# Performance work log

Measured on AMD Instinct MI355X. Metric: run time of the kernel, lower is better.

Reference implementation:

```python
import jax, jax.numpy as jnp
import numpy as np

N, IN, H, M, C, E = 200000, 256, 256, 64, 64, 3200000

def gelu(x):
    # torch F.gelu default is exact (erf) gelu
    return jax.nn.gelu(x, approximate=False)

def setup_inputs() -> dict:
    key = jax.random.key(0)
    ks = jax.random.split(key, 12)
    s = 0.02  # small init scale for weights
    p = lambda k, shape: jax.random.normal(k, shape, jnp.float32) * s
    inp = {
        "x": jax.random.normal(ks[0], (N, IN), jnp.float32),
        "edge_index": jax.random.randint(ks[1], (2, E), 0, N),
        "ff1_w0": p(ks[2], (IN, H)),   "ff1_b0": jnp.zeros((H,), jnp.float32),
        "wA0":    p(ks[3], (H, H)),    "wB0":    p(ks[4], (H, M)),
        "ff2_w0": p(ks[5], (2 * H, H)),"ff2_b0": jnp.zeros((H,), jnp.float32),
        "ff1_w1": p(ks[6], (H, H)),    "ff1_b1": jnp.zeros((H,), jnp.float32),
        "wA1":    p(ks[7], (H, H)),    "wB1":    p(ks[8], (H, M)),
        "ff2_w1": p(ks[9], (2 * H, H)),"ff2_b1": jnp.zeros((H,), jnp.float32),
        "head_w": p(ks[10], (H, C)),   "head_b": jnp.zeros((C,), jnp.float32),
    }
    return inp

def _ghm_block(X, ff1_w, ff1_b, wA, wB, ff2_w, ff2_b):
    # FF1
    Hf = gelu(X @ ff1_w + ff1_b)                 # (N, h)
    # HyperAggregation: hypernetwork produces token-mixing weights
    W_tar = gelu(Hf @ wA) @ wB                   # (N, m)
    agg = gelu(Hf.T @ W_tar)                     # (h, m) - mixes over nodes
    agg = (agg @ W_tar.T).T                      # (N, h)
    # root connection: concat aggregated with pre-agg features
    agg = gelu(jnp.concatenate([agg, Hf], axis=1))  # (N, 2h)
    return agg @ ff2_w + ff2_b                   # (N, h)

def reference(x, edge_index, ff1_w0, ff1_b0, wA0, wB0, ff2_w0, ff2_b0,
              ff1_w1, ff1_b1, wA1, wB1, ff2_w1, ff2_b1, head_w, head_b):
    # task='graph', batch=None: whole node set is one fully-connected neighborhood
    X = _ghm_block(x, ff1_w0, ff1_b0, wA0, wB0, ff2_w0, ff2_b0)
    X = _ghm_block(X, ff1_w1, ff1_b1, wA1, wB1, ff2_w1, ff2_b1)
    g = jnp.mean(X, axis=0, keepdims=True)       # (1, h)
    return g @ head_w + head_b                   # (1, C)
```

## Files before the change

### kernel.cpp

```cpp
#include <hip/hip_runtime.h>


typedef unsigned short u16;
typedef unsigned int u32;
typedef short bf16x8 __attribute__((ext_vector_type(8)));
typedef float f32x4 __attribute__((ext_vector_type(4)));

__device__ __forceinline__ float gelu_f(float x) {
  float s = x * x;
  float z = x * fmaf(s, -0.10294348f, -2.3022077f);
  float e = __builtin_amdgcn_exp2f(z);
  return x * __builtin_amdgcn_rcpf(1.0f + e);
}
__device__ __forceinline__ u16 f2b(float f) {
  union { float f; unsigned u; } v; v.f = f;
  unsigned u = v.u;
  u += 0x7fffu + ((u >> 16) & 1u);
  return (u16)(u >> 16);
}
__device__ __forceinline__ int swz(int row, int col) {
  return row * 256 + (((col >> 3) ^ (row & 7)) << 3) + (col & 7);
}

__global__ __launch_bounds__(256) void prep_weights(
    const float* __restrict__ s0, const float* __restrict__ s1,
    const float* __restrict__ s2, const float* __restrict__ s3,
    const float* __restrict__ s4, const float* __restrict__ s5,
    const float* __restrict__ s6, const float* __restrict__ s7,
    u16* __restrict__ dst)
{
  int idx = blockIdx.x * 256 + threadIdx.x;
  if (idx >= 557056) return;
  const float* src; int base, R, C;
  if (idx < 278528) {
    if (idx < 131072) {
      if (idx < 65536) { base = 0;      src = s0; R = 256; C = 256; }
      else             { base = 65536;  src = s1; R = 256; C = 256; }
    } else {
      if (idx < 147456){ base = 131072; src = s2; R = 256; C = 64;  }
      else             { base = 147456; src = s3; R = 512; C = 256; }
    }
  } else {
    int j = idx - 278528;
    if (j < 131072) {
      if (j < 65536)   { base = 278528; src = s4; R = 256; C = 256; }
      else             { base = 344064; src = s5; R = 256; C = 256; }
    } else {
      if (j < 147456)  { base = 409600; src = s6; R = 256; C = 64;  }
      else             { base = 425984; src = s7; R = 512; C = 256; }
    }
  }
  int local = idx - base;
  int o = local / R;
  int k = local - o * R;
  dst[idx] = f2b(src[k * C + o]);
}

template<bool AFP32>
__global__ __launch_bounds__(256, 2) void ff1_hyper(
    const void* __restrict__ Av, const u16* __restrict__ W1T,
    const float* __restrict__ bias, const u16* __restrict__ wAT,
    const u16* __restrict__ wBT, u16* __restrict__ Hf,
    u16* __restrict__ Hfg, u16* __restrict__ Wt, int N)
{
  __shared__ u16 Asm[128][264];
  const int tid = threadIdx.x;
  const int wave = tid >> 6, lane = tid & 63;
  int r0 = blockIdx.x * 128;
  if (r0 > N - 128) r0 = N - 128;

  if constexpr (AFP32) {
    const float* A = (const float*)Av;
    #pragma unroll
    for (int j = 0; j < 32; ++j) {
      int idx = j * 256 + tid;
      int row = idx >> 6, c4 = idx & 63;
      float4 v = *(const float4*)(A + (size_t)(r0 + row) * 256 + c4 * 4);
      uint2 p;
      p.x = (u32)f2b(v.x) | ((u32)f2b(v.y) << 16);
      p.y = (u32)f2b(v.z) | ((u32)f2b(v.w) << 16);
      *(uint2*)&Asm[row][c4 * 4] = p;
    }
  } else {
    const u16* A = (const u16*)Av;
    #pragma unroll
    for (int j = 0; j < 16; ++j) {
      int idx = j * 256 + tid;
      int row = idx >> 5, c8 = idx & 31;
      *(uint4*)&Asm[row][c8 * 8] =
          *(const uint4*)(A + (size_t)(r0 + row) * 256 + c8 * 8);
    }
  }
  __syncthreads();

  const int lm = lane & 15, lq = lane >> 4;
  const int n0 = wave * 64;

  f32x4 acc[8][4] = {};
  {
    bf16x8 bb[2][4];
    #pragma unroll
    for (int ct = 0; ct < 4; ++ct)
      bb[0][ct] = *(const bf16x8*)(W1T + (size_t)(n0 + ct * 16 + lm) * 256 + lq * 8);
    #pragma unroll
    for (int s = 0; s < 8; ++s) {
      const int cur = s & 1;
      if (s < 7)
        #pragma unroll
        for (int ct = 0; ct < 4; ++ct)
          bb[cur ^ 1][ct] = *(const bf16x8*)(W1T + (size_t)(n0 + ct * 16 + lm) * 256 + (s + 1) * 32 + lq * 8);
      bf16x8 a[8];
      #pragma unroll
      for (int rt = 0; rt < 8; ++rt)
        a[rt] = *(const bf16x8*)&Asm[rt * 16 + lm][s * 32 + lq * 8];
      #pragma unroll
      for (int rt = 0; rt < 8; ++rt)
        #pragma unroll
        for (int ct = 0; ct < 4; ++ct)
          acc[rt][ct] = __builtin_amdgcn_mfma_f32_16x16x32_bf16(a[rt], bb[cur][ct], acc[rt][ct], 0, 0, 0);
    }
  }
  __syncthreads();
  {
    float bv[4];
    #pragma unroll
    for (int ct = 0; ct < 4; ++ct) bv[ct] = bias[n0 + ct * 16 + lm];
    #pragma unroll
    for (int rt = 0; rt < 8; ++rt)
      #pragma unroll
      for (int ct = 0; ct < 4; ++ct)
        #pragma unroll
        for (int rg = 0; rg < 4; ++rg) {
          float g = gelu_f(acc[rt][ct][rg] + bv[ct]);
          u16 gb = f2b(g);
          int row = rt * 16 + lq * 4 + rg, col = n0 + ct * 16 + lm;
          size_t idx = (size_t)(r0 + row) * 256 + col;
          Hf[idx] = gb;
          Hfg[idx] = f2b(gelu_f(g));
          Asm[row][col] = gb;
        }
  }
  __syncthreads();

  #pragma unroll
  for (int rt = 0; rt < 8; ++rt)
    #pragma unroll
    for (int ct = 0; ct < 4; ++ct)
      acc[rt][ct] = (f32x4){0.f, 0.f, 0.f, 0.f};
  {
    bf16x8 bb[2][4];
    #pragma unroll
    for (int ct = 0; ct < 4; ++ct)
      bb[0][ct] = *(const bf16x8*)(wAT + (size_t)(n0 + ct * 16 + lm) * 256 + lq * 8);
    #pragma unroll
    for (int s = 0; s < 8; ++s) {
      const int cur = s & 1;
      if (s < 7)
        #pragma unroll
        for (int ct = 0; ct < 4; ++ct)
          bb[cur ^ 1][ct] = *(const bf16x8*)(wAT + (size_t)(n0 + ct * 16 + lm) * 256 + (s + 1) * 32 + lq * 8);
      bf16x8 a[8];
      #pragma unroll
      for (int rt = 0; rt < 8; ++rt)
        a[rt] = *(const bf16x8*)&Asm[rt * 16 + lm][s * 32 + lq * 8];
      #pragma unroll
      for (int rt = 0; rt < 8; ++rt)
        #pragma unroll
        for (int ct = 0; ct < 4; ++ct)
          acc[rt][ct] = __builtin_amdgcn_mfma_f32_16x16x32_bf16(a[rt], bb[cur][ct], acc[rt][ct], 0, 0, 0);
    }
  }
  __syncthreads();
  #pragma unroll
  for (int rt = 0; rt < 8; ++rt)
    #pragma unroll
    for (int ct = 0; ct < 4; ++ct)
      #pragma unroll
      for (int rg = 0; rg < 4; ++rg)
        Asm[rt * 16 + lq * 4 + rg][n0 + ct * 16 + lm] = f2b(gelu_f(acc[rt][ct][rg]));
  __syncthreads();

  f32x4 acc2[2][4] = {};
  {
    bf16x8 bb[2][4];
    #pragma unroll
    for (int ct = 0; ct < 4; ++ct)
      bb[0][ct] = *(const bf16x8*)(wBT + (size_t)(ct * 16 + lm) * 256 + lq * 8);
    #pragma unroll
    for (int s = 0; s < 8; ++s) {
      const int cur = s & 1;
      if (s < 7)
        #pragma unroll
        for (int ct = 0; ct < 4; ++ct)
          bb[cur ^ 1][ct] = *(const bf16x8*)(wBT + (size_t)(ct * 16 + lm) * 256 + (s + 1) * 32 + lq * 8);
      bf16x8 a[2];
      #pragma unroll
      for (int rt = 0; rt < 2; ++rt)
        a[rt] = *(const bf16x8*)&Asm[wave * 32 + rt * 16 + lm][s * 32 + lq * 8];
      #pragma unroll
      for (int rt = 0; rt < 2; ++rt)
        #pragma unroll
        for (int ct = 0; ct < 4; ++ct)
          acc2[rt][ct] = __builtin_amdgcn_mfma_f32_16x16x32_bf16(a[rt], bb[cur][ct], acc2[rt][ct], 0, 0, 0);
    }
  }
  #pragma unroll
  for (int rt = 0; rt < 2; ++rt)
    #pragma unroll
    for (int ct = 0; ct < 4; ++ct)
      #pragma unroll
      for (int rg = 0; rg < 4; ++rg)
        Wt[(size_t)(r0 + wave * 32 + rt * 16 + lq * 4 + rg) * 64 + ct * 16 + lm] =
            f2b(acc2[rt][ct][rg]);
}

__global__ __launch_bounds__(256) void s_partial_v2(
    const u16* __restrict__ Hf, const u16* __restrict__ Wt,
    float* __restrict__ Spart, int N)
{
  __shared__ u16 HfT[256][72];
  __shared__ u16 WtT[64][72];
  const int tid = threadIdx.x;
  const int wave = tid >> 6, lane = tid & 63;
  const int lm = lane & 15, lq = lane >> 4;
  const int rp = tid & 31;
  const int mb = tid >> 5;
  uint4 hx[4][2], wx[2];
  auto issue = [&](int ch) {
    int i0 = ch << 6;
    #pragma unroll
    for (int q = 0; q < 4; ++q) {
      const u16* px = Hf + (size_t)(i0 + 2 * rp) * 256 + (mb + 8 * q) * 8;
      hx[q][0] = *(const uint4*)px;
      hx[q][1] = *(const uint4*)(px + 256);
    }
    const u16* pw = Wt + (size_t)(i0 + 2 * rp) * 64 + mb * 8;
    wx[0] = *(const uint4*)pw;
    wx[1] = *(const uint4*)(pw + 64);
  };
  f32x4 acc[4][4] = {};
  const int nchunk = N >> 6;
  int ch = blockIdx.x;
  if (ch < nchunk) issue(ch);
  for (; ch < nchunk; ch += gridDim.x) {
    __syncthreads();
    #pragma unroll
    for (int q = 0; q < 4; ++q) {
      int m = mb + 8 * q;
      u32 xs[4] = {hx[q][0].x, hx[q][0].y, hx[q][0].z, hx[q][0].w};
      u32 ys[4] = {hx[q][1].x, hx[q][1].y, hx[q][1].z, hx[q][1].w};
      #pragma unroll
      for (int t = 0; t < 4; ++t) {
        *(u32*)&HfT[m * 8 + 2 * t][2 * rp]     = (xs[t] & 0xFFFFu) | (ys[t] << 16);
        *(u32*)&HfT[m * 8 + 2 * t + 1][2 * rp] = (xs[t] >> 16) | (ys[t] & 0xFFFF0000u);
      }
    }
    {
      u32 xs[4] = {wx[0].x, wx[0].y, wx[0].z, wx[0].w};
      u32 ys[4] = {wx[1].x, wx[1].y, wx[1].z, wx[1].w};
      #pragma unroll
      for (int t = 0; t < 4; ++t) {
        *(u32*)&WtT[mb * 8 + 2 * t][2 * rp]     = (xs[t] & 0xFFFFu) | (ys[t] << 16);
        *(u32*)&WtT[mb * 8 + 2 * t + 1][2 * rp] = (xs[t] >> 16) | (ys[t] & 0xFFFF0000u);
      }
    }
    __syncthreads();
    if (ch + (int)gridDim.x < nchunk) issue(ch + (int)gridDim.x);
    #pragma unroll
    for (int k0 = 0; k0 < 64; k0 += 32) {
      bf16x8 a[4], b[4];
      #pragma unroll
      for (int t = 0; t < 4; ++t)
        a[t] = *(const bf16x8*)&HfT[wave * 64 + t * 16 + lm][k0 + lq * 8];
      #pragma unroll
      for (int m = 0; m < 4; ++m)
        b[m] = *(const bf16x8*)&WtT[m * 16 + lm][k0 + lq * 8];
      #pragma unroll
      for (int t = 0; t < 4; ++t)
        #pragma unroll
        for (int m = 0; m < 4; ++m)
          acc[t][m] = __builtin_amdgcn_mfma_f32_16x16x32_bf16(a[t], b[m], acc[t][m], 0, 0, 0);
    }
  }
  float* out = Spart + (size_t)blockIdx.x * 16384;
  #pragma unroll
  for (int t = 0; t < 4; ++t)
    #pragma unroll
    for (int m = 0; m < 4; ++m)
      #pragma unroll
      for (int rg = 0; rg < 4; ++rg)
        out[(size_t)(wave * 64 + t * 16 + lq * 4 + rg) * 64 + m * 16 + lm] = acc[t][m][rg];
}

__global__ __launch_bounds__(256) void s_reduce(
    const float* __restrict__ Spart, u16* __restrict__ agg, int nparts)
{
  int e = blockIdx.x * 256 + threadIdx.x;
  float s0 = 0.f, s1 = 0.f, s2 = 0.f, s3 = 0.f;
  for (int p = 0; p < nparts; p += 4) {
    s0 += Spart[(size_t)(p + 0) * 16384 + e];
    s1 += Spart[(size_t)(p + 1) * 16384 + e];
    s2 += Spart[(size_t)(p + 2) * 16384 + e];
    s3 += Spart[(size_t)(p + 3) * 16384 + e];
  }
  agg[e] = f2b(gelu_f((s0 + s1) + (s2 + s3)));
}

template<bool COLSUM>
__global__ __launch_bounds__(256, 2) void fused_p_ff2_v6(
    const u16* __restrict__ Wt, const u16* __restrict__ agg,
    const u16* __restrict__ Hfg, const u16* __restrict__ W2T,
    const float* __restrict__ bias, u16* __restrict__ X,
    float* __restrict__ colsum, int N)
{
  __shared__ u16 Hsm[64 * 256];
  __shared__ u16 Pl[64 * 256];
  const int tid = threadIdx.x;
  const int wave = tid >> 6, lane = tid & 63;
  const int lm = lane & 15, lq = lane >> 4;
  const int r0 = blockIdx.x * 64;
  const int n0 = wave * 64;

  #pragma unroll
  for (int t = 0; t < 8; ++t) {
    int unit = (wave * 8 + t) * 64 + lane;
    int row = unit >> 5, ksw = unit & 31;
    int kc = ksw ^ (row & 7);
    const u16* g = Hfg + (size_t)(r0 + row) * 256 + kc * 8;
    __builtin_amdgcn_global_load_lds(
        (const __attribute__((address_space(1))) void*)g,
        (__attribute__((address_space(3))) void*)(Hsm + (size_t)(wave * 8 + t) * 512),
        16, 0, 0);
  }

  {
    f32x4 acc[4][4] = {};
    #pragma unroll
    for (int k0 = 0; k0 < 64; k0 += 32) {
      bf16x8 a[4], b[4];
      #pragma unroll
      for (int ct = 0; ct < 4; ++ct)
        b[ct] = *(const bf16x8*)(agg + (size_t)(n0 + ct * 16 + lm) * 64 + k0 + lq * 8);
      #pragma unroll
      for (int rt = 0; rt < 4; ++rt)
        a[rt] = *(const bf16x8*)(Wt + (size_t)(r0 + rt * 16 + lm) * 64 + k0 + lq * 8);
      #pragma unroll
      for (int rt = 0; rt < 4; ++rt)
        #pragma unroll
        for (int ct = 0; ct < 4; ++ct)
          acc[rt][ct] = __builtin_amdgcn_mfma_f32_16x16x32_bf16(a[rt], b[ct], acc[rt][ct], 0, 0, 0);
    }
    #pragma unroll
    for (int rt = 0; rt < 4; ++rt)
      #pragma unroll
      for (int ct = 0; ct < 4; ++ct)
        #pragma unroll
        for (int rg = 0; rg < 4; ++rg)
          Pl[swz(rt * 16 + lq * 4 + rg, n0 + ct * 16 + lm)] = f2b(gelu_f(acc[rt][ct][rg]));
  }
  __syncthreads();

  auto ldb = [&](int s, bf16x8* b) {
    #pragma unroll
    for (int ct = 0; ct < 4; ++ct)
      b[ct] = *(const bf16x8*)(W2T + (size_t)(n0 + ct * 16 + lm) * 512 + s * 32 + lq * 8);
  };
  auto lda = [&](int s, bf16x8* a) {
    const u16* base = (s < 8) ? Pl : Hsm;
    const int k0 = (s & 7) * 32;
    #pragma unroll
    for (int rt = 0; rt < 4; ++rt) {
      int row = rt * 16 + lm;
      a[rt] = *(const bf16x8*)&base[swz(row, k0 + lq * 8)];
    }
  };
  f32x4 acc[4][4] = {};
  bf16x8 ab[2][4], bb[2][4];
  ldb(0, bb[0]);
  lda(0, ab[0]);
  #pragma unroll
  for (int s = 0; s < 16; ++s) {
    const int cur = s & 1, nxt = cur ^ 1;
    if (s < 15) { ldb(s + 1, bb[nxt]); lda(s + 1, ab[nxt]); }
    #pragma unroll
    for (int rt = 0; rt < 4; ++rt)
      #pragma unroll
      for (int ct = 0; ct < 4; ++ct)
        acc[rt][ct] = __builtin_amdgcn_mfma_f32_16x16x32_bf16(ab[cur][rt], bb[cur][ct], acc[rt][ct], 0, 0, 0);
  }
  float bv[4];
  #pragma unroll
  for (int ct = 0; ct < 4; ++ct) bv[ct] = bias[n0 + ct * 16 + lm];
  if constexpr (!COLSUM) {
    #pragma unroll
    for (int rt = 0; rt < 4; ++rt)
      #pragma unroll
      for (int ct = 0; ct < 4; ++ct)
        #pragma unroll
        for (int rg = 0; rg < 4; ++rg)
          X[(size_t)(r0 + rt * 16 + lq * 4 + rg) * 256 + n0 + ct * 16 + lm] =
              f2b(acc[rt][ct][rg] + bv[ct]);
  } else {
    #pragma unroll
    for (int ct = 0; ct < 4; ++ct) {
      float cs = 0.0f;
      #pragma unroll
      for (int rt = 0; rt < 4; ++rt)
        #pragma unroll
        for (int rg = 0; rg < 4; ++rg) cs += acc[rt][ct][rg] + bv[ct];
      cs += __shfl_down(cs, 32);
      cs += __shfl_down(cs, 16);
      if (lq == 0) atomicAdd(&colsum[n0 + ct * 16 + lm], cs);
    }
  }
}

__global__ __launch_bounds__(64) void head_kernel(
    const float* __restrict__ colsum, const float* __restrict__ head_w,
    const float* __restrict__ head_b, float* __restrict__ out, float invN)
{
  const int c = threadIdx.x;
  float s = head_b[c];
  for (int h = 0; h < 256; ++h) s = fmaf(colsum[h] * invN, head_w[h * 64 + c], s);
  out[c] = s;
}

extern "C" void kernel_launch(void* const* d_in, const int* in_sizes, int n_in,
                              void* d_out, int out_size, void* d_ws, size_t ws_size,
                              hipStream_t stream)
{
  const float* x        = (const float*)d_in[0];
  const float* ff1_w[2] = {(const float*)d_in[2],  (const float*)d_in[8]};
  const float* ff1_b[2] = {(const float*)d_in[3],  (const float*)d_in[9]};
  const float* wA[2]    = {(const float*)d_in[4],  (const float*)d_in[10]};
  const float* wB[2]    = {(const float*)d_in[5],  (const float*)d_in[11]};
  const float* ff2_w[2] = {(const float*)d_in[6],  (const float*)d_in[12]};
  const float* ff2_b[2] = {(const float*)d_in[7],  (const float*)d_in[13]};
  const float* head_w   = (const float*)d_in[14];
  const float* head_b   = (const float*)d_in[15];
  const int N = in_sizes[0] / 256;

  char* ws = (char*)d_ws;
  u16* WT = (u16*)ws;
  u16* W1T[2] = {WT + 0,      WT + 278528};
  u16* wAT[2] = {WT + 65536,  WT + 344064};
  u16* wBT[2] = {WT + 131072, WT + 409600};
  u16* W2T[2] = {WT + 147456, WT + 425984};
  size_t o = 1114112;
  u16* Hf  = (u16*)(ws + o); o += (size_t)N * 256 * 2;
  u16* Hfg = (u16*)(ws + o); o += (size_t)N * 256 * 2;
  u16* TX  = (u16*)(ws + o); o += (size_t)N * 256 * 2;
  u16* Wt  = (u16*)(ws + o); o += (size_t)N * 64 * 2;
  float* Spart  = (float*)(ws + o); o += (size_t)512 * 16384 * 4;
  u16*   agg    = (u16*)(ws + o);   o += 16384 * 2;
  float* colsum = (float*)(ws + o); o += 256 * 4;
  (void)ws_size; (void)n_in; (void)out_size;

  hipMemsetAsync(colsum, 0, 256 * sizeof(float), stream);
  prep_weights<<<2176, 256, 0, stream>>>(ff1_w[0], wA[0], wB[0], ff2_w[0],
                                         ff1_w[1], wA[1], wB[1], ff2_w[1], WT);
  const int G128 = (N + 127) / 128;
  const int G64  = N / 64;
  ff1_hyper<true><<<G128, 256, 0, stream>>>(x, W1T[0], ff1_b[0], wAT[0], wBT[0], Hf, Hfg, Wt, N);
  s_partial_v2<<<512, 256, 0, stream>>>(Hf, Wt, Spart, N);
  s_reduce<<<64, 256, 0, stream>>>(Spart, agg, 512);
  fused_p_ff2_v6<false><<<G64, 256, 0, stream>>>(Wt, agg, Hfg, W2T[0], ff2_b[0], TX, nullptr, N);
  ff1_hyper<false><<<G128, 256, 0, stream>>>(TX, W1T[1], ff1_b[1], wAT[1], wBT[1], Hf, Hfg, Wt, N);
  s_partial_v2<<<512, 256, 0, stream>>>(Hf, Wt, Spart, N);
  s_reduce<<<64, 256, 0, stream>>>(Spart, agg, 512);
  fused_p_ff2_v6<true><<<G64, 256, 0, stream>>>(Wt, agg, Hfg, W2T[1], ff2_b[1], nullptr, colsum, N);
  head_kernel<<<1, 64, 0, stream>>>(colsum, head_w, head_b, (float*)d_out, 1.0f / (float)N);
}
```

Measured before the change: 1.221 ms.

## Fuse Hf^T·W_tar partial reduction into FF1/hyper kernel, drop Hf buffer

```diff
diff --git a/kernel.cpp b/kernel.cpp
--- a/kernel.cpp
+++ b/kernel.cpp
@@ -57,239 +57,188 @@
 }
 
 template<bool AFP32>
-__global__ __launch_bounds__(256, 2) void ff1_hyper(
+__global__ __launch_bounds__(256, 2) void ff1_hyper_s(
     const void* __restrict__ Av, const u16* __restrict__ W1T,
     const float* __restrict__ bias, const u16* __restrict__ wAT,
-    const u16* __restrict__ wBT, u16* __restrict__ Hf,
-    u16* __restrict__ Hfg, u16* __restrict__ Wt, int N)
-{
-  __shared__ u16 Asm[128][264];
-  const int tid = threadIdx.x;
-  const int wave = tid >> 6, lane = tid & 63;
-  int r0 = blockIdx.x * 128;
-  if (r0 > N - 128) r0 = N - 128;
-
-  if constexpr (AFP32) {
-    const float* A = (const float*)Av;
-    #pragma unroll
-    for (int j = 0; j < 32; ++j) {
-      int idx = j * 256 + tid;
-      int row = idx >> 6, c4 = idx & 63;
-      float4 v = *(const float4*)(A + (size_t)(r0 + row) * 256 + c4 * 4);
-      uint2 p;
-      p.x = (u32)f2b(v.x) | ((u32)f2b(v.y) << 16);
-      p.y = (u32)f2b(v.z) | ((u32)f2b(v.w) << 16);
-      *(uint2*)&Asm[row][c4 * 4] = p;
-    }
-  } else {
-    const u16* A = (const u16*)Av;
-    #pragma unroll
-    for (int j = 0; j < 16; ++j) {
-      int idx = j * 256 + tid;
-      int row = idx >> 5, c8 = idx & 31;
-      *(uint4*)&Asm[row][c8 * 8] =
-          *(const uint4*)(A + (size_t)(r0 + row) * 256 + c8 * 8);
-    }
-  }
-  __syncthreads();
-
-  const int lm = lane & 15, lq = lane >> 4;
-  const int n0 = wave * 64;
-
-  f32x4 acc[8][4] = {};
-  {
-    bf16x8 bb[2][4];
-    #pragma unroll
-    for (int ct = 0; ct < 4; ++ct)
-      bb[0][ct] = *(const bf16x8*)(W1T + (size_t)(n0 + ct * 16 + lm) * 256 + lq * 8);
-    #pragma unroll
-    for (int s = 0; s < 8; ++s) {
-      const int cur = s & 1;
-      if (s < 7)
-        #pragma unroll
-        for (int ct = 0; ct < 4; ++ct)
-          bb[cur ^ 1][ct] = *(const bf16x8*)(W1T + (size_t)(n0 + ct * 16 + lm) * 256 + (s + 1) * 32 + lq * 8);
-      bf16x8 a[8];
-      #pragma unroll
-      for (int rt = 0; rt < 8; ++rt)
-        a[rt] = *(const bf16x8*)&Asm[rt * 16 + lm][s * 32 + lq * 8];
-      #pragma unroll
-      for (int rt = 0; rt < 8; ++rt)
-        #pragma unroll
-        for (int ct = 0; ct < 4; ++ct)
-          acc[rt][ct] = __builtin_amdgcn_mfma_f32_16x16x32_bf16(a[rt], bb[cur][ct], acc[rt][ct], 0, 0, 0);
-    }
-  }
-  __syncthreads();
-  {
-    float bv[4];
-    #pragma unroll
-    for (int ct = 0; ct < 4; ++ct) bv[ct] = bias[n0 + ct * 16 + lm];
-    #pragma unroll
-    for (int rt = 0; rt < 8; ++rt)
-      #pragma unroll
-      for (int ct = 0; ct < 4; ++ct)
-        #pragma unroll
-        for (int rg = 0; rg < 4; ++rg) {
-          float g = gelu_f(acc[rt][ct][rg] + bv[ct]);
-          u16 gb = f2b(g);
-          int row = rt * 16 + lq * 4 + rg, col = n0 + ct * 16 + lm;
-          size_t idx = (size_t)(r0 + row) * 256 + col;
-          Hf[idx] = gb;
-          Hfg[idx] = f2b(gelu_f(g));
-          Asm[row][col] = gb;
-        }
-  }
-  __syncthreads();
-
-  #pragma unroll
-  for (int rt = 0; rt < 8; ++rt)
-    #pragma unroll
-    for (int ct = 0; ct < 4; ++ct)
-      acc[rt][ct] = (f32x4){0.f, 0.f, 0.f, 0.f};
-  {
-    bf16x8 bb[2][4];
-    #pragma unroll
-    for (int ct = 0; ct < 4; ++ct)
-      bb[0][ct] = *(const bf16x8*)(wAT + (size_t)(n0 + ct * 16 + lm) * 256 + lq * 8);
-    #pragma unroll
-    for (int s = 0; s < 8; ++s) {
-      const int cur = s & 1;
-      if (s < 7)
-        #pragma unroll
-        for (int ct = 0; ct < 4; ++ct)
-          bb[cur ^ 1][ct] = *(const bf16x8*)(wAT + (size_t)(n0 + ct * 16 + lm) * 256 + (s + 1) * 32 + lq * 8);
-      bf16x8 a[8];
-      #pragma unroll
-      for (int rt = 0; rt < 8; ++rt)
-        a[rt] = *(const bf16x8*)&Asm[rt * 16 + lm][s * 32 + lq * 8];
-      #pragma unroll
-      for (int rt = 0; rt < 8; ++rt)
-        #pragma unroll
-        for (int ct = 0; ct < 4; ++ct)
-          acc[rt][ct] = __builtin_amdgcn_mfma_f32_16x16x32_bf16(a[rt], bb[cur][ct], acc[rt][ct], 0, 0, 0);
-    }
-  }
-  __syncthreads();
-  #pragma unroll
-  for (int rt = 0; rt < 8; ++rt)
-    #pragma unroll
-    for (int ct = 0; ct < 4; ++ct)
-      #pragma unroll
-      for (int rg = 0; rg < 4; ++rg)
-        Asm[rt * 16 + lq * 4 + rg][n0 + ct * 16 + lm] = f2b(gelu_f(acc[rt][ct][rg]));
-  __syncthreads();
-
-  f32x4 acc2[2][4] = {};
-  {
-    bf16x8 bb[2][4];
-    #pragma unroll
-    for (int ct = 0; ct < 4; ++ct)
-      bb[0][ct] = *(const bf16x8*)(wBT + (size_t)(ct * 16 + lm) * 256 + lq * 8);
-    #pragma unroll
-    for (int s = 0; s < 8; ++s) {
-      const int cur = s & 1;
-      if (s < 7)
-        #pragma unroll
-        for (int ct = 0; ct < 4; ++ct)
-          bb[cur ^ 1][ct] = *(const bf16x8*)(wBT + (size_t)(ct * 16 + lm) * 256 + (s + 1) * 32 + lq * 8);
-      bf16x8 a[2];
-      #pragma unroll
-      for (int rt = 0; rt < 2; ++rt)
-        a[rt] = *(const bf16x8*)&Asm[wave * 32 + rt * 16 + lm][s * 32 + lq * 8];
-      #pragma unroll
-      for (int rt = 0; rt < 2; ++rt)
-        #pragma unroll
-        for (int ct = 0; ct < 4; ++ct)
-          acc2[rt][ct] = __builtin_amdgcn_mfma_f32_16x16x32_bf16(a[rt], bb[cur][ct], acc2[rt][ct], 0, 0, 0);
-    }
-  }
-  #pragma unroll
-  for (int rt = 0; rt < 2; ++rt)
-    #pragma unroll
-    for (int ct = 0; ct < 4; ++ct)
-      #pragma unroll
-      for (int rg = 0; rg < 4; ++rg)
-        Wt[(size_t)(r0 + wave * 32 + rt * 16 + lq * 4 + rg) * 64 + ct * 16 + lm] =
-            f2b(acc2[rt][ct][rg]);
-}
-
-__global__ __launch_bounds__(256) void s_partial_v2(
-    const u16* __restrict__ Hf, const u16* __restrict__ Wt,
-    float* __restrict__ Spart, int N)
-{
-  __shared__ u16 HfT[256][72];
+    const u16* __restrict__ wBT, u16* __restrict__ Hfg,
+    u16* __restrict__ Wt, float* __restrict__ Spart, int N)
+{
+  __shared__ u16 Asm[64][264];
+  __shared__ u16 Tsm[64][264];
   __shared__ u16 WtT[64][72];
   const int tid = threadIdx.x;
   const int wave = tid >> 6, lane = tid & 63;
   const int lm = lane & 15, lq = lane >> 4;
-  const int rp = tid & 31;
-  const int mb = tid >> 5;
-  uint4 hx[4][2], wx[2];
-  auto issue = [&](int ch) {
-    int i0 = ch << 6;
-    #pragma unroll
-    for (int q = 0; q < 4; ++q) {
-      const u16* px = Hf + (size_t)(i0 + 2 * rp) * 256 + (mb + 8 * q) * 8;
-      hx[q][0] = *(const uint4*)px;
-      hx[q][1] = *(const uint4*)(px + 256);
-    }
-    const u16* pw = Wt + (size_t)(i0 + 2 * rp) * 64 + mb * 8;
-    wx[0] = *(const uint4*)pw;
-    wx[1] = *(const uint4*)(pw + 64);
-  };
-  f32x4 acc[4][4] = {};
-  const int nchunk = N >> 6;
-  int ch = blockIdx.x;
-  if (ch < nchunk) issue(ch);
-  for (; ch < nchunk; ch += gridDim.x) {
-    __syncthreads();
-    #pragma unroll
-    for (int q = 0; q < 4; ++q) {
-      int m = mb + 8 * q;
-      u32 xs[4] = {hx[q][0].x, hx[q][0].y, hx[q][0].z, hx[q][0].w};
-      u32 ys[4] = {hx[q][1].x, hx[q][1].y, hx[q][1].z, hx[q][1].w};
-      #pragma unroll
-      for (int t = 0; t < 4; ++t) {
-        *(u32*)&HfT[m * 8 + 2 * t][2 * rp]     = (xs[t] & 0xFFFFu) | (ys[t] << 16);
-        *(u32*)&HfT[m * 8 + 2 * t + 1][2 * rp] = (xs[t] >> 16) | (ys[t] & 0xFFFF0000u);
-      }
-    }
+  const int n0 = wave * 64;
+  const int ntiles = N >> 6;
+
+  float bv[4];
+  #pragma unroll
+  for (int ct = 0; ct < 4; ++ct) bv[ct] = bias[n0 + ct * 16 + lm];
+
+  f32x4 accS[4][4] = {};
+
+  for (int tile = blockIdx.x; tile < ntiles; tile += (int)gridDim.x) {
+    const int r0 = tile << 6;
+
+    if constexpr (AFP32) {
+      const float* A = (const float*)Av;
+      #pragma unroll
+      for (int j = 0; j < 16; ++j) {
+        int idx = j * 256 + tid;
+        int row = idx >> 6, c4 = idx & 63;
+        float4 v = *(const float4*)(A + (size_t)(r0 + row) * 256 + c4 * 4);
+        uint2 p;
+        p.x = (u32)f2b(v.x) | ((u32)f2b(v.y) << 16);
+        p.y = (u32)f2b(v.z) | ((u32)f2b(v.w) << 16);
+        *(uint2*)&Asm[row][c4 * 4] = p;
+      }
+    } else {
+      const u16* A = (const u16*)Av;
+      #pragma unroll
+      for (int j = 0; j < 8; ++j) {
+        int idx = j * 256 + tid;
+        int row = idx >> 5, c8 = idx & 31;
+        *(uint4*)&Asm[row][c8 * 8] =
+            *(const uint4*)(A + (size_t)(r0 + row) * 256 + c8 * 8);
+      }
+    }
+    __syncthreads();
+
+    f32x4 acc[4][4] = {};
     {
-      u32 xs[4] = {wx[0].x, wx[0].y, wx[0].z, wx[0].w};
-      u32 ys[4] = {wx[1].x, wx[1].y, wx[1].z, wx[1].w};
-      #pragma unroll
-      for (int t = 0; t < 4; ++t) {
-        *(u32*)&WtT[mb * 8 + 2 * t][2 * rp]     = (xs[t] & 0xFFFFu) | (ys[t] << 16);
-        *(u32*)&WtT[mb * 8 + 2 * t + 1][2 * rp] = (xs[t] >> 16) | (ys[t] & 0xFFFF0000u);
-      }
-    }
-    __syncthreads();
-    if (ch + (int)gridDim.x < nchunk) issue(ch + (int)gridDim.x);
+      bf16x8 bb[2][4];
+      #pragma unroll
+      for (int ct = 0; ct < 4; ++ct)
+        bb[0][ct] = *(const bf16x8*)(W1T + (size_t)(n0 + ct * 16 + lm) * 256 + lq * 8);
+      #pragma unroll
+      for (int s = 0; s < 8; ++s) {
+        const int cur = s & 1;
+        if (s < 7)
+          #pragma unroll
+          for (int ct = 0; ct < 4; ++ct)
+            bb[cur ^ 1][ct] = *(const bf16x8*)(W1T + (size_t)(n0 + ct * 16 + lm) * 256 + (s + 1) * 32 + lq * 8);
+        bf16x8 a[4];
+        #pragma unroll
+        for (int rt = 0; rt < 4; ++rt)
+          a[rt] = *(const bf16x8*)&Asm[rt * 16 + lm][s * 32 + lq * 8];
+        #pragma unroll
+        for (int rt = 0; rt < 4; ++rt)
+          #pragma unroll
+          for (int ct = 0; ct < 4; ++ct)
+            acc[rt][ct] = __builtin_amdgcn_mfma_f32_16x16x32_bf16(a[rt], bb[cur][ct], acc[rt][ct], 0, 0, 0);
+      }
+    }
+    __syncthreads();
+
+    #pragma unroll
+    for (int rt = 0; rt < 4; ++rt)
+      #pragma unroll
+      for (int ct = 0; ct < 4; ++ct)
+        #pragma unroll
+        for (int rg = 0; rg < 4; ++rg) {
+          float g = gelu_f(acc[rt][ct][rg] + bv[ct]);
+          int row = rt * 16 + lq * 4 + rg, col = n0 + ct * 16 + lm;
+          Asm[row][col] = f2b(g);
+          Hfg[(size_t)(r0 + row) * 256 + col] = f2b(gelu_f(g));
+        }
+    __syncthreads();
+
+    #pragma unroll
+    for (int rt = 0; rt < 4; ++rt)
+      #pragma unroll
+      for (int ct = 0; ct < 4; ++ct)
+        acc[rt][ct] = (f32x4){0.f, 0.f, 0.f, 0.f};
+    {
+      bf16x8 bb[2][4];
+      #pragma unroll
+      for (int ct = 0; ct < 4; ++ct)
+        bb[0][ct] = *(const bf16x8*)(wAT + (size_t)(n0 + ct * 16 + lm) * 256 + lq * 8);
+      #pragma unroll
+      for (int s = 0; s < 8; ++s) {
+        const int cur = s & 1;
+        if (s < 7)
+          #pragma unroll
+          for (int ct = 0; ct < 4; ++ct)
+            bb[cur ^ 1][ct] = *(const bf16x8*)(wAT + (size_t)(n0 + ct * 16 + lm) * 256 + (s + 1) * 32 + lq * 8);
+        bf16x8 a[4];
+        #pragma unroll
+        for (int rt = 0; rt < 4; ++rt)
+          a[rt] = *(const bf16x8*)&Asm[rt * 16 + lm][s * 32 + lq * 8];
+        #pragma unroll
+        for (int rt = 0; rt < 4; ++rt)
+          #pragma unroll
+          for (int ct = 0; ct < 4; ++ct)
+            acc[rt][ct] = __builtin_amdgcn_mfma_f32_16x16x32_bf16(a[rt], bb[cur][ct], acc[rt][ct], 0, 0, 0);
+      }
+    }
+    #pragma unroll
+    for (int rt = 0; rt < 4; ++rt)
+      #pragma unroll
+      for (int ct = 0; ct < 4; ++ct)
+        #pragma unroll
+        for (int rg = 0; rg < 4; ++rg)
+          Tsm[rt * 16 + lq * 4 + rg][n0 + ct * 16 + lm] = f2b(gelu_f(acc[rt][ct][rg]));
+    __syncthreads();
+
+    f32x4 acc2[4] = {};
+    {
+      bf16x8 bb[2][4];
+      #pragma unroll
+      for (int ct = 0; ct < 4; ++ct)
+        bb[0][ct] = *(const bf16x8*)(wBT + (size_t)(ct * 16 + lm) * 256 + lq * 8);
+      #pragma unroll
+      for (int s = 0; s < 8; ++s) {
+        const int cur = s & 1;
+        if (s < 7)
+          #pragma unroll
+          for (int ct = 0; ct < 4; ++ct)
+            bb[cur ^ 1][ct] = *(const bf16x8*)(wBT + (size_t)(ct * 16 + lm) * 256 + (s + 1) * 32 + lq * 8);
+        bf16x8 a0 = *(const bf16x8*)&Tsm[wave * 16 + lm][s * 32 + lq * 8];
+        #pragma unroll
+        for (int ct = 0; ct < 4; ++ct)
+          acc2[ct] = __builtin_amdgcn_mfma_f32_16x16x32_bf16(a0, bb[cur][ct], acc2[ct], 0, 0, 0);
+      }
+    }
+    #pragma unroll
+    for (int ct = 0; ct < 4; ++ct)
+      #pragma unroll
+      for (int rg = 0; rg < 4; ++rg) {
+        u16 vb = f2b(acc2[ct][rg]);
+        int row = wave * 16 + lq * 4 + rg, m = ct * 16 + lm;
+        Wt[(size_t)(r0 + row) * 64 + m] = vb;
+        WtT[m][row] = vb;
+      }
+    __syncthreads();
+
     #pragma unroll
     for (int k0 = 0; k0 < 64; k0 += 32) {
-      bf16x8 a[4], b[4];
-      #pragma unroll
-      for (int t = 0; t < 4; ++t)
-        a[t] = *(const bf16x8*)&HfT[wave * 64 + t * 16 + lm][k0 + lq * 8];
-      #pragma unroll
-      for (int m = 0; m < 4; ++m)
-        b[m] = *(const bf16x8*)&WtT[m * 16 + lm][k0 + lq * 8];
-      #pragma unroll
-      for (int t = 0; t < 4; ++t)
-        #pragma unroll
-        for (int m = 0; m < 4; ++m)
-          acc[t][m] = __builtin_amdgcn_mfma_f32_16x16x32_bf16(a[t], b[m], acc[t][m], 0, 0, 0);
-    }
-  }
+      bf16x8 b[4];
+      #pragma unroll
+      for (int mt = 0; mt < 4; ++mt)
+        b[mt] = *(const bf16x8*)&WtT[mt * 16 + lm][k0 + lq * 8];
+      #pragma unroll
+      for (int ht = 0; ht < 4; ++ht) {
+        bf16x8 a;
+        #pragma unroll
+        for (int e = 0; e < 8; ++e)
+          a[e] = (short)Asm[k0 + lq * 8 + e][n0 + ht * 16 + lm];
+        #pragma unroll
+        for (int mt = 0; mt < 4; ++mt)
+          accS[ht][mt] = __builtin_amdgcn_mfma_f32_16x16x32_bf16(a, b[mt], accS[ht][mt], 0, 0, 0);
+      }
+    }
+    __syncthreads();
+  }
+
   float* out = Spart + (size_t)blockIdx.x * 16384;
   #pragma unroll
-  for (int t = 0; t < 4; ++t)
-    #pragma unroll
-    for (int m = 0; m < 4; ++m)
+  for (int ht = 0; ht < 4; ++ht)
+    #pragma unroll
+    for (int mt = 0; mt < 4; ++mt)
       #pragma unroll
       for (int rg = 0; rg < 4; ++rg)
-        out[(size_t)(wave * 64 + t * 16 + lq * 4 + rg) * 64 + m * 16 + lm] = acc[t][m][rg];
+        out[(size_t)(n0 + ht * 16 + lq * 4 + rg) * 64 + mt * 16 + lm] = accS[ht][mt][rg];
 }
 
 __global__ __launch_bounds__(256) void s_reduce(
@@ -333,33 +282,6 @@
         16, 0, 0);
   }
 
-  {
-    f32x4 acc[4][4] = {};
-    #pragma unroll
-    for (int k0 = 0; k0 < 64; k0 += 32) {
-      bf16x8 a[4], b[4];
-      #pragma unroll
-      for (int ct = 0; ct < 4; ++ct)
-        b[ct] = *(const bf16x8*)(agg + (size_t)(n0 + ct * 16 + lm) * 64 + k0 + lq * 8);
-      #pragma unroll
-      for (int rt = 0; rt < 4; ++rt)
-        a[rt] = *(const bf16x8*)(Wt + (size_t)(r0 + rt * 16 + lm) * 64 + k0 + lq * 8);
-      #pragma unroll
-      for (int rt = 0; rt < 4; ++rt)
-        #pragma unroll
-        for (int ct = 0; ct < 4; ++ct)
-          acc[rt][ct] = __builtin_amdgcn_mfma_f32_16x16x32_bf16(a[rt], b[ct], acc[rt][ct], 0, 0, 0);
-    }
-    #pragma unroll
-    for (int rt = 0; rt < 4; ++rt)
-      #pragma unroll
-      for (int ct = 0; ct < 4; ++ct)
-        #pragma unroll
-        for (int rg = 0; rg < 4; ++rg)
-          Pl[swz(rt * 16 + lq * 4 + rg, n0 + ct * 16 + lm)] = f2b(gelu_f(acc[rt][ct][rg]));
-  }
-  __syncthreads();
-
   auto ldb = [&](int s, bf16x8* b) {
     #pragma unroll
     for (int ct = 0; ct < 4; ++ct)
@@ -374,19 +296,51 @@
       a[rt] = *(const bf16x8*)&base[swz(row, k0 + lq * 8)];
     }
   };
+
+  bf16x8 bb[3][4];
+  ldb(0, bb[0]);
+  ldb(1, bb[1]);
+
+  {
+    f32x4 acc[4][4] = {};
+    #pragma unroll
+    for (int k0 = 0; k0 < 64; k0 += 32) {
+      bf16x8 a[4], b[4];
+      #pragma unroll
+      for (int ct = 0; ct < 4; ++ct)
+        b[ct] = *(const bf16x8*)(agg + (size_t)(n0 + ct * 16 + lm) * 64 + k0 + lq * 8);
+      #pragma unroll
+      for (int rt = 0; rt < 4; ++rt)
+        a[rt] = *(const bf16x8*)(Wt + (size_t)(r0 + rt * 16 + lm) * 64 + k0 + lq * 8);
+      #pragma unroll
+      for (int rt = 0; rt < 4; ++rt)
+        #pragma unroll
+        for (int ct = 0; ct < 4; ++ct)
+          acc[rt][ct] = __builtin_amdgcn_mfma_f32_16x16x32_bf16(a[rt], b[ct], acc[rt][ct], 0, 0, 0);
+    }
+    #pragma unroll
+    for (int rt = 0; rt < 4; ++rt)
+      #pragma unroll
+      for (int ct = 0; ct < 4; ++ct)
+        #pragma unroll
+        for (int rg = 0; rg < 4; ++rg)
+          Pl[swz(rt * 16 + lq * 4 + rg, n0 + ct * 16 + lm)] = f2b(gelu_f(acc[rt][ct][rg]));
+  }
+  __syncthreads();
+
   f32x4 acc[4][4] = {};
-  bf16x8 ab[2][4], bb[2][4];
-  ldb(0, bb[0]);
+  bf16x8 ab[2][4];
   lda(0, ab[0]);
   #pragma unroll
   for (int s = 0; s < 16; ++s) {
     const int cur = s & 1, nxt = cur ^ 1;
-    if (s < 15) { ldb(s + 1, bb[nxt]); lda(s + 1, ab[nxt]); }
-    #pragma unroll
-    for (int rt = 0; rt < 4; ++rt)
-      #pragma unroll
-      for (int ct = 0; ct < 4; ++ct)
-        acc[rt][ct] = __builtin_amdgcn_mfma_f32_16x16x32_bf16(ab[cur][rt], bb[cur][ct], acc[rt][ct], 0, 0, 0);
+    if (s < 14) ldb(s + 2, bb[(s + 2) % 3]);
+    if (s < 15) lda(s + 1, ab[nxt]);
+    #pragma unroll
+    for (int rt = 0; rt < 4; ++rt)
+      #pragma unroll
+      for (int ct = 0; ct < 4; ++ct)
+        acc[rt][ct] = __builtin_amdgcn_mfma_f32_16x16x32_bf16(ab[cur][rt], bb[s % 3][ct], acc[rt][ct], 0, 0, 0);
   }
   float bv[4];
   #pragma unroll
@@ -447,7 +401,6 @@
   u16* wBT[2] = {WT + 131072, WT + 409600};
   u16* W2T[2] = {WT + 147456, WT + 425984};
   size_t o = 1114112;
-  u16* Hf  = (u16*)(ws + o); o += (size_t)N * 256 * 2;
   u16* Hfg = (u16*)(ws + o); o += (size_t)N * 256 * 2;
   u16* TX  = (u16*)(ws + o); o += (size_t)N * 256 * 2;
   u16* Wt  = (u16*)(ws + o); o += (size_t)N * 64 * 2;
@@ -459,14 +412,11 @@
   hipMemsetAsync(colsum, 0, 256 * sizeof(float), stream);
   prep_weights<<<2176, 256, 0, stream>>>(ff1_w[0], wA[0], wB[0], ff2_w[0],
                                          ff1_w[1], wA[1], wB[1], ff2_w[1], WT);
-  const int G128 = (N + 127) / 128;
-  const int G64  = N / 64;
-  ff1_hyper<true><<<G128, 256, 0, stream>>>(x, W1T[0], ff1_b[0], wAT[0], wBT[0], Hf, Hfg, Wt, N);
-  s_partial_v2<<<512, 256, 0, stream>>>(Hf, Wt, Spart, N);
+  const int G64 = N / 64;
+  ff1_hyper_s<true><<<512, 256, 0, stream>>>(x, W1T[0], ff1_b[0], wAT[0], wBT[0], Hfg, Wt, Spart, N);
   s_reduce<<<64, 256, 0, stream>>>(Spart, agg, 512);
   fused_p_ff2_v6<false><<<G64, 256, 0, stream>>>(Wt, agg, Hfg, W2T[0], ff2_b[0], TX, nullptr, N);
-  ff1_hyper<false><<<G128, 256, 0, stream>>>(TX, W1T[1], ff1_b[1], wAT[1], wBT[1], Hf, Hfg, Wt, N);
-  s_partial_v2<<<512, 256, 0, stream>>>(Hf, Wt, Spart, N);
+  ff1_hyper_s<false><<<512, 256, 0, stream>>>(TX, W1T[1], ff1_b[1], wAT[1], wBT[1], Hfg, Wt, Spart, N);
   s_reduce<<<64, 256, 0, stream>>>(Spart, agg, 512);
   fused_p_ff2_v6<true><<<G64, 256, 0, stream>>>(Wt, agg, Hfg, W2T[1], ff2_b[1], nullptr, colsum, N);
   head_kernel<<<1, 64, 0, stream>>>(colsum, head_w, head_b, (float*)d_out, 1.0f / (float)N);
```

After: 1.430 ms. 17.1% more time.

## Stage Hf/Hfg/Wt stores through LDS for coalesced writes; deepen W2 prefetch

Applied to the files above, without the earlier changes.

```diff
diff --git a/kernel.cpp b/kernel.cpp
--- a/kernel.cpp
+++ b/kernel.cpp
@@ -17,6 +17,10 @@
   unsigned u = v.u;
   u += 0x7fffu + ((u >> 16) & 1u);
   return (u16)(u >> 16);
+}
+__device__ __forceinline__ float b2f(u16 b) {
+  union { float f; u32 u; } v; v.u = (u32)b << 16;
+  return v.f;
 }
 __device__ __forceinline__ int swz(int row, int col) {
   return row * 256 + (((col >> 3) ^ (row & 7)) << 3) + (col & 7);
@@ -121,6 +125,7 @@
     }
   }
   __syncthreads();
+
   {
     float bv[4];
     #pragma unroll
@@ -132,15 +137,28 @@
         #pragma unroll
         for (int rg = 0; rg < 4; ++rg) {
           float g = gelu_f(acc[rt][ct][rg] + bv[ct]);
-          u16 gb = f2b(g);
-          int row = rt * 16 + lq * 4 + rg, col = n0 + ct * 16 + lm;
-          size_t idx = (size_t)(r0 + row) * 256 + col;
-          Hf[idx] = gb;
-          Hfg[idx] = f2b(gelu_f(g));
-          Asm[row][col] = gb;
+          Asm[rt * 16 + lq * 4 + rg][n0 + ct * 16 + lm] = f2b(g);
         }
   }
   __syncthreads();
+
+  #pragma unroll
+  for (int j = 0; j < 16; ++j) {
+    int idx = j * 256 + tid;
+    int row = idx >> 5, c8 = idx & 31;
+    uint4 v = *(const uint4*)&Asm[row][c8 * 8];
+    *(uint4*)(Hf + (size_t)(r0 + row) * 256 + c8 * 8) = v;
+    u32 wsv[4] = {v.x, v.y, v.z, v.w};
+    uint4 go;
+    u32* gp = (u32*)&go;
+    #pragma unroll
+    for (int t = 0; t < 4; ++t) {
+      float lo = gelu_f(b2f((u16)(wsv[t] & 0xFFFFu)));
+      float hi = gelu_f(b2f((u16)(wsv[t] >> 16)));
+      gp[t] = (u32)f2b(lo) | ((u32)f2b(hi) << 16);
+    }
+    *(uint4*)(Hfg + (size_t)(r0 + row) * 256 + c8 * 8) = go;
+  }
 
   #pragma unroll
   for (int rt = 0; rt < 8; ++rt)
@@ -210,8 +228,14 @@
     for (int ct = 0; ct < 4; ++ct)
       #pragma unroll
       for (int rg = 0; rg < 4; ++rg)
-        Wt[(size_t)(r0 + wave * 32 + rt * 16 + lq * 4 + rg) * 64 + ct * 16 + lm] =
-            f2b(acc2[rt][ct][rg]);
+        Asm[wave * 32 + rt * 16 + lq * 4 + rg][ct * 16 + lm] = f2b(acc2[rt][ct][rg]);
+  #pragma unroll
+  for (int t = 0; t < 4; ++t) {
+    int u = t * 64 + lane;
+    int rl = u >> 3, c8 = u & 7;
+    *(uint4*)(Wt + (size_t)(r0 + wave * 32 + rl) * 64 + c8 * 8) =
+        *(const uint4*)&Asm[wave * 32 + rl][c8 * 8];
+  }
 }
 
 __global__ __launch_bounds__(256) void s_partial_v2(
@@ -333,33 +357,6 @@
         16, 0, 0);
   }
 
-  {
-    f32x4 acc[4][4] = {};
-    #pragma unroll
-    for (int k0 = 0; k0 < 64; k0 += 32) {
-      bf16x8 a[4], b[4];
-      #pragma unroll
-      for (int ct = 0; ct < 4; ++ct)
-        b[ct] = *(const bf16x8*)(agg + (size_t)(n0 + ct * 16 + lm) * 64 + k0 + lq * 8);
-      #pragma unroll
-      for (int rt = 0; rt < 4; ++rt)
-        a[rt] = *(const bf16x8*)(Wt + (size_t)(r0 + rt * 16 + lm) * 64 + k0 + lq * 8);
-      #pragma unroll
-      for (int rt = 0; rt < 4; ++rt)
-        #pragma unroll
-        for (int ct = 0; ct < 4; ++ct)
-          acc[rt][ct] = __builtin_amdgcn_mfma_f32_16x16x32_bf16(a[rt], b[ct], acc[rt][ct], 0, 0, 0);
-    }
-    #pragma unroll
-    for (int rt = 0; rt < 4; ++rt)
-      #pragma unroll
-      for (int ct = 0; ct < 4; ++ct)
-        #pragma unroll
-        for (int rg = 0; rg < 4; ++rg)
-          Pl[swz(rt * 16 + lq * 4 + rg, n0 + ct * 16 + lm)] = f2b(gelu_f(acc[rt][ct][rg]));
-  }
-  __syncthreads();
-
   auto ldb = [&](int s, bf16x8* b) {
     #pragma unroll
     for (int ct = 0; ct < 4; ++ct)
@@ -374,19 +371,51 @@
       a[rt] = *(const bf16x8*)&base[swz(row, k0 + lq * 8)];
     }
   };
+
+  bf16x8 bb[3][4];
+  ldb(0, bb[0]);
+  ldb(1, bb[1]);
+
+  {
+    f32x4 acc[4][4] = {};
+    #pragma unroll
+    for (int k0 = 0; k0 < 64; k0 += 32) {
+      bf16x8 a[4], b[4];
+      #pragma unroll
+      for (int ct = 0; ct < 4; ++ct)
+        b[ct] = *(const bf16x8*)(agg + (size_t)(n0 + ct * 16 + lm) * 64 + k0 + lq * 8);
+      #pragma unroll
+      for (int rt = 0; rt < 4; ++rt)
+        a[rt] = *(const bf16x8*)(Wt + (size_t)(r0 + rt * 16 + lm) * 64 + k0 + lq * 8);
+      #pragma unroll
+      for (int rt = 0; rt < 4; ++rt)
+        #pragma unroll
+        for (int ct = 0; ct < 4; ++ct)
+          acc[rt][ct] = __builtin_amdgcn_mfma_f32_16x16x32_bf16(a[rt], b[ct], acc[rt][ct], 0, 0, 0);
+    }
+    #pragma unroll
+    for (int rt = 0; rt < 4; ++rt)
+      #pragma unroll
+      for (int ct = 0; ct < 4; ++ct)
+        #pragma unroll
+        for (int rg = 0; rg < 4; ++rg)
+          Pl[swz(rt * 16 + lq * 4 + rg, n0 + ct * 16 + lm)] = f2b(gelu_f(acc[rt][ct][rg]));
+  }
+  __syncthreads();
+
   f32x4 acc[4][4] = {};
-  bf16x8 ab[2][4], bb[2][4];
-  ldb(0, bb[0]);
+  bf16x8 ab[2][4];
   lda(0, ab[0]);
   #pragma unroll
   for (int s = 0; s < 16; ++s) {
     const int cur = s & 1, nxt = cur ^ 1;
-    if (s < 15) { ldb(s + 1, bb[nxt]); lda(s + 1, ab[nxt]); }
+    if (s < 14) ldb(s + 2, bb[(s + 2) % 3]);
+    if (s < 15) lda(s + 1, ab[nxt]);
     #pragma unroll
     for (int rt = 0; rt < 4; ++rt)
       #pragma unroll
       for (int ct = 0; ct < 4; ++ct)
-        acc[rt][ct] = __builtin_amdgcn_mfma_f32_16x16x32_bf16(ab[cur][rt], bb[cur][ct], acc[rt][ct], 0, 0, 0);
+        acc[rt][ct] = __builtin_amdgcn_mfma_f32_16x16x32_bf16(ab[cur][rt], bb[s % 3][ct], acc[rt][ct], 0, 0, 0);
   }
   float bv[4];
   #pragma unroll
```

After: 1.074 ms. 12.1% less time.
